# Performance work log

Measured on AMD Instinct MI355X. Metric: run time of the kernel, lower is better.

Reference implementation:

```python
import jax, jax.numpy as jnp
import numpy as np

B, L, D_IN, D_MODEL, D_STATE, N_LAYERS = 16, 2048, 64, 512, 16, 4
LN_EPS = 1e-5


def setup_inputs() -> dict:
    key = jax.random.key(0)
    ks = jax.random.split(key, 16)
    s = 0.02
    x = jax.random.normal(ks[0], (B, L, D_IN), jnp.float32)
    W_in0 = jax.random.normal(ks[1], (D_IN, D_MODEL), jnp.float32) * s
    b_in0 = jnp.zeros((D_MODEL,), jnp.float32)
    W_in = jax.random.normal(ks[2], (N_LAYERS - 1, D_MODEL, D_MODEL), jnp.float32) * s
    b_in = jnp.zeros((N_LAYERS - 1, D_MODEL), jnp.float32)
    # S4D-style init: A_log = log(1..N) per channel
    A_log = jnp.broadcast_to(jnp.log(jnp.arange(1, D_STATE + 1, dtype=jnp.float32)), (N_LAYERS, D_MODEL, D_STATE)).copy()
    D_skip = jnp.ones((N_LAYERS, D_MODEL), jnp.float32)
    W_dt = jax.random.normal(ks[3], (N_LAYERS, D_MODEL, D_MODEL), jnp.float32) * s
    b_dt = jnp.full((N_LAYERS, D_MODEL), -4.0, jnp.float32)  # small initial dt
    W_B = jax.random.normal(ks[4], (N_LAYERS, D_MODEL, D_STATE), jnp.float32) * s
    W_C = jax.random.normal(ks[5], (N_LAYERS, D_MODEL, D_STATE), jnp.float32) * s
    ln_g = jnp.ones((D_MODEL,), jnp.float32)
    ln_b = jnp.zeros((D_MODEL,), jnp.float32)
    head_w = jax.random.normal(ks[6], (D_MODEL, 1), jnp.float32) * s
    head_b = jnp.zeros((1,), jnp.float32)
    return {"x": x, "W_in0": W_in0, "b_in0": b_in0, "W_in": W_in, "b_in": b_in,
            "A_log": A_log, "D_skip": D_skip, "W_dt": W_dt, "b_dt": b_dt,
            "W_B": W_B, "W_C": W_C, "ln_g": ln_g, "ln_b": ln_b,
            "head_w": head_w, "head_b": head_b}


def _mamba_layer(x, W_in_l, b_in_l, A_log_l, D_l, W_dt_l, b_dt_l, W_B_l, W_C_l):
    # x: (B, L, d_in) -> y: (B, L, D_MODEL)
    u = x @ W_in_l + b_in_l                    # (B, L, D)
    dt = jax.nn.softplus(u @ W_dt_l + b_dt_l)  # (B, L, D)
    Bm = u @ W_B_l                             # (B, L, N)
    Cm = u @ W_C_l                             # (B, L, N)
    A = -jnp.exp(A_log_l)                      # (D, N)

    def step(h, inp):
        dt_t, u_t, B_t, C_t = inp              # (B,D),(B,D),(B,N),(B,N)
        dA = jnp.exp(dt_t[..., None] * A)      # (B, D, N)
        h = dA * h + (dt_t * u_t)[..., None] * B_t[:, None, :]
        y_t = jnp.einsum('bdn,bn->bd', h, C_t)
        return h, y_t

    h0 = jnp.zeros((u.shape[0], u.shape[2], A.shape[1]), u.dtype)
    xs = (jnp.swapaxes(dt, 0, 1), jnp.swapaxes(u, 0, 1),
          jnp.swapaxes(Bm, 0, 1), jnp.swapaxes(Cm, 0, 1))
    _, ys = jax.lax.scan(step, h0, xs)         # ys: (L, B, D)
    return jnp.swapaxes(ys, 0, 1) + u * D_l


def reference(x, W_in0, b_in0, W_in, b_in, A_log, D_skip, W_dt, b_dt, W_B, W_C, ln_g, ln_b, head_w, head_b):
    h = x
    for i in range(N_LAYERS):
        Wi = W_in0 if i == 0 else W_in[i - 1]
        bi = b_in0 if i == 0 else b_in[i - 1]
        h = _mamba_layer(h, Wi, bi, A_log[i], D_skip[i], W_dt[i], b_dt[i], W_B[i], W_C[i])
    # LayerNorm over d_model
    mu = jnp.mean(h, axis=-1, keepdims=True)
    var = jnp.mean(jnp.square(h - mu), axis=-1, keepdims=True)
    h = (h - mu) * jax.lax.rsqrt(var + LN_EPS) * ln_g + ln_b
    return h[:, -1, :] @ head_w + head_b       # (B, 1)
```

## Files before the change

kernel.cpp:

```cpp
#include <hip/hip_runtime.h>
#include <hip/hip_bf16.h>
#include <cstdint>
#include <cstddef>

#define B_SZ    16
#define L_SZ    2048
#define DIN     64
#define DMODEL  512
#define DSTATE  16
#define NLAYERS 4
#define LN_EPS  1e-5f
#define NC      32
#define TCH     (L_SZ / NC)
#define NFUSED  (2 * DMODEL)

typedef __bf16 bf16x8 __attribute__((ext_vector_type(8)));
typedef float  f32x4  __attribute__((ext_vector_type(4)));
typedef unsigned short u16;
typedef unsigned int   u32;

__device__ __forceinline__ u16 f2bf(float f) {
    u32 u = __builtin_bit_cast(u32, f);
    u += 0x7fffu + ((u >> 16) & 1u);
    return (u16)(u >> 16);
}
__device__ __forceinline__ float bf2f(u16 v) {
    u32 u = ((u32)v) << 16;
    return __builtin_bit_cast(float, u);
}

__device__ __forceinline__ void pow16(float q, float* a_) {
    float q2 = q * q, q4 = q2 * q2, q8 = q4 * q4;
    a_[0] = q;        a_[1] = q2;       a_[2] = q2 * q;   a_[3] = q4;
    a_[4] = q4 * q;   a_[5] = q4 * q2;  a_[6] = a_[5] * q; a_[7] = q8;
    a_[8] = q8 * q;   a_[9] = q8 * q2;  a_[10] = a_[9] * q; a_[11] = q8 * q4;
    a_[12] = a_[11] * q; a_[13] = a_[11] * q2; a_[14] = a_[13] * q; a_[15] = q8 * q8;
}

#define LOG2E 1.4426950408889634f

__device__ __forceinline__ void gload16(const void* g, void* l) {
    __builtin_amdgcn_global_load_lds(
        (__attribute__((address_space(1))) void*)(g),
        (__attribute__((address_space(3))) void*)(l), 16, 0, 0);
}

template <int K>
__global__ __launch_bounds__(256) void gemm_fused(
    const u16* __restrict__ A, const u16* __restrict__ BT,
    const float* __restrict__ bias, u16* __restrict__ Cu,
    u16* __restrict__ Cdt, int M)
{
    constexpr int BM = 128, BK = 64;
    constexpr int NT = K / BK;
    __shared__ u16 As[2][BM * BK];
    __shared__ u16 Bs[2][BM * BK];

    const int tid = threadIdx.x;
    const int wv = tid >> 6, ln = tid & 63;
    const int bm = blockIdx.x * BM, bn = blockIdx.y * BM;
    const int wm = (wv >> 1) * 64, wn = (wv & 1) * 64;

    f32x4 acc[4][4];
#pragma unroll
    for (int i = 0; i < 4; ++i)
#pragma unroll
        for (int j = 0; j < 4; ++j) acc[i][j] = (f32x4){0.f, 0.f, 0.f, 0.f};

    auto stage = [&](int buf, int k0) {
#pragma unroll
        for (int i = 0; i < 4; ++i) {
            int t = i * 256 + tid;
            int m = t >> 3, s = t & 7;
            int ksrc = (s ^ (m & 7)) * 8;
            gload16(A + (size_t)(bm + m) * K + k0 + ksrc,
                    &As[buf][(i * 256 + wv * 64) * 8]);
            gload16(BT + (size_t)(bn + m) * K + k0 + ksrc,
                    &Bs[buf][(i * 256 + wv * 64) * 8]);
        }
    };

    stage(0, 0);
    if (NT > 1) stage(1, BK);

#pragma unroll
    for (int kt = 0; kt < NT; ++kt) {
        if (kt == NT - 1) asm volatile("s_waitcnt vmcnt(0)" ::: "memory");
        else              asm volatile("s_waitcnt vmcnt(8)" ::: "memory");
        __builtin_amdgcn_s_barrier();

        const int buf = kt & 1;
#pragma unroll
        for (int ks = 0; ks < 2; ++ks) {
            bf16x8 af[4], bfr[4];
            const int g = ln >> 4, lm = ln & 15;
            const int c = ks * 4 + g;
#pragma unroll
            for (int f = 0; f < 4; ++f) {
                int ml = wm + f * 16 + lm;
                af[f] = *(const bf16x8*)&As[buf][ml * 64 + ((c ^ (ml & 7)) * 8)];
                int nl = wn + f * 16 + lm;
                bfr[f] = *(const bf16x8*)&Bs[buf][nl * 64 + ((c ^ (nl & 7)) * 8)];
            }
#pragma unroll
            for (int fm = 0; fm < 4; ++fm)
#pragma unroll
                for (int fn = 0; fn < 4; ++fn)
                    acc[fm][fn] = __builtin_amdgcn_mfma_f32_16x16x32_bf16(
                        af[fm], bfr[fn], acc[fm][fn], 0, 0, 0);
        }

        asm volatile("s_waitcnt lgkmcnt(0)" ::: "memory");
        __builtin_amdgcn_s_barrier();
        if (kt + 2 < NT) stage(buf, (kt + 2) * BK);
    }

    const int cg = ln >> 4, lc = ln & 15;
    const bool uside = (bn < DMODEL);
#pragma unroll
    for (int fm = 0; fm < 4; ++fm) {
#pragma unroll
        for (int fn = 0; fn < 4; ++fn) {
            int col = bn + wn + fn * 16 + lc;
            float bv = bias[col];
#pragma unroll
            for (int r = 0; r < 4; ++r) {
                int row = bm + wm + fm * 16 + cg * 4 + r;
                float v = acc[fm][fn][r] + bv;
                if (uside) {
                    Cu[(size_t)row * DMODEL + col] = f2bf(v);
                } else {
                    v = (v > 20.f) ? v : __logf(1.f + __expf(v));
                    Cdt[(size_t)row * DMODEL + (col - DMODEL)] = f2bf(v);
                }
            }
        }
    }
}

__global__ __launch_bounds__(256) void wtrans(
    const float* __restrict__ W, u16* __restrict__ WT, int K, int N)
{
    __shared__ float tile[32][33];
    int k0 = blockIdx.x * 32, n0 = blockIdx.y * 32;
    int tx = threadIdx.x & 31, ty = threadIdx.x >> 5;
#pragma unroll
    for (int i = 0; i < 4; ++i)
        tile[ty + 8 * i][tx] = W[(size_t)(k0 + ty + 8 * i) * N + n0 + tx];
    __syncthreads();
#pragma unroll
    for (int i = 0; i < 4; ++i)
        WT[(size_t)(n0 + ty + 8 * i) * K + k0 + tx] = f2bf(tile[tx][ty + 8 * i]);
}

__global__ __launch_bounds__(256) void wcombo(
    const float* __restrict__ Win,
    const float* __restrict__ Wdt,
    u16* __restrict__ outT,
    int KD)
{
    __shared__ float wi[16][516];
    __shared__ float wd[512][16];
    const int k0 = blockIdx.x * 16, n0 = blockIdx.y * 16;
    const int tid = threadIdx.x;
    for (int i = tid; i < 16 * 128; i += 256) {
        int r = i >> 7, c = i & 127;
        *(float4*)&wi[r][c * 4] =
            *(const float4*)&Win[(size_t)(k0 + r) * DMODEL + c * 4];
    }
    for (int i = tid; i < 512 * 4; i += 256) {
        int j = i >> 2, c = i & 3;
        *(float4*)&wd[j][c * 4] =
            *(const float4*)&Wdt[(size_t)j * DMODEL + n0 + c * 4];
    }
    __syncthreads();
    const int kk = tid & 15, nn = tid >> 4;
    float acc = 0.f;
#pragma unroll 8
    for (int j = 0; j < 512; ++j)
        acc = fmaf(wi[kk][j], wd[j][nn], acc);
    outT[(size_t)(n0 + nn) * KD + k0 + kk] = f2bf(acc);
}

__global__ __launch_bounds__(256) void biasprep(
    const float* __restrict__ bin, const float* __restrict__ Wdt,
    const float* __restrict__ bdt, float* __restrict__ biascat)
{
    int idx = blockIdx.x * 256 + threadIdx.x;
    if (idx < DMODEL) { biascat[idx] = bin[idx]; return; }
    int n = idx - DMODEL;
    float acc = bdt[n];
    for (int j = 0; j < DMODEL; ++j)
        acc = fmaf(bin[j], Wdt[(size_t)j * DMODEL + n], acc);
    biascat[idx] = acc;
}

__global__ __launch_bounds__(256) void castx(
    const float* __restrict__ x, u16* __restrict__ xb, int n4)
{
    int i = blockIdx.x * 256 + threadIdx.x;
    if (i < n4) {
        float4 v = ((const float4*)x)[i];
        ushort4 o;
        o.x = f2bf(v.x); o.y = f2bf(v.y); o.z = f2bf(v.z); o.w = f2bf(v.w);
        ((ushort4*)xb)[i] = o;
    }
}

__global__ __launch_bounds__(256) void prep_wbc(
    const float* __restrict__ WB, const float* __restrict__ WC,
    u16* __restrict__ WBCT)
{
    int idx = blockIdx.x * 256 + threadIdx.x;
    int l = idx >> 14;
    int r = idx & 16383;
    int n = r >> 9, k = r & 511;
    float v = (n < 16) ? WB[((size_t)l * DMODEL + k) * DSTATE + n]
                       : WC[((size_t)l * DMODEL + k) * DSTATE + (n - 16)];
    WBCT[((size_t)l * 32 + n) * DMODEL + k] = f2bf(v);
}

__global__ __launch_bounds__(256) void gemm_bc_mfma(
    const u16* __restrict__ A, const u16* __restrict__ WBCT,
    float* __restrict__ Bo, float* __restrict__ Co)
{
    const int tid = threadIdx.x;
    const int wv = tid >> 6, ln = tid & 63;
    const int m0 = blockIdx.x * 64 + wv * 16;
    const int g = ln >> 4, lm = ln & 15;

    f32x4 accB = (f32x4){0.f, 0.f, 0.f, 0.f};
    f32x4 accC = (f32x4){0.f, 0.f, 0.f, 0.f};
    const u16* arow = A + (size_t)(m0 + lm) * DMODEL;
    const u16* wb = WBCT + (size_t)lm * DMODEL;
    const u16* wc = WBCT + (size_t)(lm + 16) * DMODEL;
#pragma unroll
    for (int ks = 0; ks < DMODEL / 32; ++ks) {
        int ko = ks * 32 + g * 8;
        bf16x8 a = *(const bf16x8*)&arow[ko];
        bf16x8 b = *(const bf16x8*)&wb[ko];
        bf16x8 c = *(const bf16x8*)&wc[ko];
        accB = __builtin_amdgcn_mfma_f32_16x16x32_bf16(a, b, accB, 0, 0, 0);
        accC = __builtin_amdgcn_mfma_f32_16x16x32_bf16(a, c, accC, 0, 0, 0);
    }
#pragma unroll
    for (int r = 0; r < 4; ++r) {
        int m = m0 + g * 4 + r;
        Bo[(size_t)m * DSTATE + lm] = accB[r];
        Co[(size_t)m * DSTATE + lm] = accC[r];
    }
}

__global__ __launch_bounds__(256) void scan_pass1(
    const u16* __restrict__ u, const u16* __restrict__ dt,
    const float* __restrict__ Bm, const float* __restrict__ A_log,
    float* __restrict__ P, float* __restrict__ S)
{
    const int tid = threadIdx.x;
    const int d = blockIdx.x * 256 + tid;
    const int c = blockIdx.y, b = blockIdx.z;
    __shared__ float Bs[TCH][DSTATE];

    const float* Bsrc = Bm + ((size_t)b * L_SZ + (size_t)c * TCH) * DSTATE;
    for (int i = tid; i < TCH * DSTATE / 4; i += 256)
        ((float4*)Bs)[i] = ((const float4*)Bsrc)[i];

    float Ac[16];
#pragma unroll
    for (int n = 0; n < 16; ++n) Ac[n] = -__expf(A_log[d * DSTATE + n]);
    bool geo = true;
#pragma unroll
    for (int n = 1; n < 16; ++n)
        geo &= fabsf(Ac[n] - (n + 1) * Ac[0]) <= 1e-4f * (n + 1) * fabsf(Ac[0]);
    __syncthreads();

    float s[16];
#pragma unroll
    for (int n = 0; n < 16; ++n) s[n] = 0.f;

    const size_t base = ((size_t)b * L_SZ + (size_t)c * TCH) * DMODEL + d;
    size_t o = (((size_t)b * NC + c) * DMODEL + d) * DSTATE;

    if (geo) {
        const float cK = Ac[0] * LOG2E;
        float qp = 1.f;
#pragma unroll 2
        for (int t = 0; t < TCH; ++t) {
            float dtv = bf2f(dt[base + (size_t)t * DMODEL]);
            float uv  = bf2f(u [base + (size_t)t * DMODEL]);
            float du = dtv * uv;
            float q = exp2f(dtv * cK);
            qp *= q;
            float a_[16];
            pow16(q, a_);
#pragma unroll
            for (int n = 0; n < 16; ++n)
                s[n] = fmaf(a_[n], s[n], du * Bs[t][n]);
        }
        float p_[16];
        pow16(qp, p_);
#pragma unroll
        for (int n = 0; n < 16; ++n) { P[o + n] = p_[n]; S[o + n] = s[n]; }
    } else {
        float p[16];
#pragma unroll
        for (int n = 0; n < 16; ++n) p[n] = 1.f;
#pragma unroll 2
        for (int t = 0; t < TCH; ++t) {
            float dtv = bf2f(dt[base + (size_t)t * DMODEL]);
            float uv  = bf2f(u [base + (size_t)t * DMODEL]);
            float du = dtv * uv;
#pragma unroll
            for (int n = 0; n < 16; ++n) {
                float a = __expf(dtv * Ac[n]);
                p[n] *= a;
                s[n] = fmaf(a, s[n], du * Bs[t][n]);
            }
        }
#pragma unroll
        for (int n = 0; n < 16; ++n) { P[o + n] = p[n]; S[o + n] = s[n]; }
    }
}

__global__ __launch_bounds__(256) void scan_fix(
    const float* __restrict__ P, const float* __restrict__ S,
    float* __restrict__ H0)
{
    const int idx = blockIdx.x * 256 + threadIdx.x;
    const int dn = idx & (DMODEL * DSTATE - 1);
    const int b = idx >> 13;
    float h = 0.f;
#pragma unroll
    for (int c = 0; c < NC; ++c) {
        size_t o = (((size_t)b * NC + c) << 13) + dn;
        H0[o] = h;
        h = fmaf(P[o], h, S[o]);
    }
}

__global__ __launch_bounds__(256) void scan_pass2(
    const u16* __restrict__ u, const u16* __restrict__ dt,
    const float* __restrict__ Bm, const float* __restrict__ Cm,
    const float* __restrict__ A_log, const float* __restrict__ Dskip,
    const float* __restrict__ H0, u16* __restrict__ yb,
    float* __restrict__ ylast)
{
    const int tid = threadIdx.x;
    const int d = blockIdx.x * 256 + tid;
    const int c = blockIdx.y, b = blockIdx.z;
    __shared__ float Bs[TCH][DSTATE];
    __shared__ float Cs[TCH][DSTATE];

    const float* Bsrc = Bm + ((size_t)b * L_SZ + (size_t)c * TCH) * DSTATE;
    const float* Csrc = Cm + ((size_t)b * L_SZ + (size_t)c * TCH) * DSTATE;
    for (int i = tid; i < TCH * DSTATE / 4; i += 256) {
        ((float4*)Bs)[i] = ((const float4*)Bsrc)[i];
        ((float4*)Cs)[i] = ((const float4*)Csrc)[i];
    }

    float Ac[16];
#pragma unroll
    for (int n = 0; n < 16; ++n) Ac[n] = -__expf(A_log[d * DSTATE + n]);
    bool geo = true;
#pragma unroll
    for (int n = 1; n < 16; ++n)
        geo &= fabsf(Ac[n] - (n + 1) * Ac[0]) <= 1e-4f * (n + 1) * fabsf(Ac[0]);
    const float Dk = Dskip[d];

    float h[16];
    size_t ho = (((size_t)b * NC + c) * DMODEL + d) * DSTATE;
#pragma unroll
    for (int n = 0; n < 16; ++n) h[n] = H0[ho + n];
    __syncthreads();

    const size_t base = ((size_t)b * L_SZ + (size_t)c * TCH) * DMODEL + d;

    if (geo) {
        const float cK = Ac[0] * LOG2E;
#pragma unroll 2
        for (int t = 0; t < TCH; ++t) {
            float dtv = bf2f(dt[base + (size_t)t * DMODEL]);
            float uv  = bf2f(u [base + (size_t)t * DMODEL]);
            float du = dtv * uv;
            float q = exp2f(dtv * cK);
            float a_[16];
            pow16(q, a_);
            float yv = 0.f;
#pragma unroll
            for (int n = 0; n < 16; ++n) {
                h[n] = fmaf(a_[n], h[n], du * Bs[t][n]);
                yv = fmaf(h[n], Cs[t][n], yv);
            }
            yv = fmaf(uv, Dk, yv);
            yb[base + (size_t)t * DMODEL] = f2bf(yv);
            if (c == NC - 1 && t == TCH - 1) ylast[(size_t)b * DMODEL + d] = yv;
        }
    } else {
#pragma unroll 2
        for (int t = 0; t < TCH; ++t) {
            float dtv = bf2f(dt[base + (size_t)t * DMODEL]);
            float uv  = bf2f(u [base + (size_t)t * DMODEL]);
            float du = dtv * uv;
            float yv = 0.f;
#pragma unroll
            for (int n = 0; n < 16; ++n) {
                float a = __expf(dtv * Ac[n]);
                h[n] = fmaf(a, h[n], du * Bs[t][n]);
                yv = fmaf(h[n], Cs[t][n], yv);
            }
            yv = fmaf(uv, Dk, yv);
            yb[base + (size_t)t * DMODEL] = f2bf(yv);
            if (c == NC - 1 && t == TCH - 1) ylast[(size_t)b * DMODEL + d] = yv;
        }
    }
}

__global__ __launch_bounds__(256) void ln_head_kernel(
    const float* __restrict__ ylast, const float* __restrict__ g,
    const float* __restrict__ bb, const float* __restrict__ hw,
    const float* __restrict__ hb, float* __restrict__ out)
{
    const int b = blockIdx.x;
    const int tid = threadIdx.x;
    const float* row = ylast + (size_t)b * DMODEL;
    float v0 = row[tid], v1 = row[tid + 256];
    float s = v0 + v1;
    float s2 = v0 * v0 + v1 * v1;
#pragma unroll
    for (int o = 32; o >= 1; o >>= 1) {
        s += __shfl_xor(s, o);
        s2 += __shfl_xor(s2, o);
    }
    __shared__ float red[8];
    const int w = tid >> 6;
    if ((tid & 63) == 0) { red[w] = s; red[4 + w] = s2; }
    __syncthreads();
    s = red[0] + red[1] + red[2] + red[3];
    s2 = red[4] + red[5] + red[6] + red[7];
    float mu = s * (1.f / DMODEL);
    float var = s2 * (1.f / DMODEL) - mu * mu;
    float r = rsqrtf(var + LN_EPS);
    float c = ((v0 - mu) * r * g[tid] + bb[tid]) * hw[tid]
            + ((v1 - mu) * r * g[tid + 256] + bb[tid + 256]) * hw[tid + 256];
#pragma unroll
    for (int o = 32; o >= 1; o >>= 1) c += __shfl_xor(c, o);
    __syncthreads();
    if ((tid & 63) == 0) red[w] = c;
    __syncthreads();
    if (tid == 0) out[b] = red[0] + red[1] + red[2] + red[3] + hb[0];
}

extern "C" void kernel_launch(void* const* d_in, const int* in_sizes, int n_in,
                              void* d_out, int out_size, void* d_ws, size_t ws_size,
                              hipStream_t stream)
{
    const float* x      = (const float*)d_in[0];
    const float* W_in0  = (const float*)d_in[1];
    const float* b_in0  = (const float*)d_in[2];
    const float* W_in   = (const float*)d_in[3];
    const float* b_in   = (const float*)d_in[4];
    const float* A_log  = (const float*)d_in[5];
    const float* D_skip = (const float*)d_in[6];
    const float* W_dt   = (const float*)d_in[7];
    const float* b_dt   = (const float*)d_in[8];
    const float* W_B    = (const float*)d_in[9];
    const float* W_C    = (const float*)d_in[10];
    const float* ln_g   = (const float*)d_in[11];
    const float* ln_b   = (const float*)d_in[12];
    const float* head_w = (const float*)d_in[13];
    const float* head_b = (const float*)d_in[14];
    float* out = (float*)d_out;

    const size_t BLD = (size_t)B_SZ * L_SZ * DMODEL;
    const size_t BLN = (size_t)B_SZ * L_SZ * DSTATE;
    const size_t BCD = (size_t)B_SZ * NC * DMODEL * DSTATE;
    const size_t XBN = (size_t)B_SZ * L_SZ * DIN;

    float* fp = (float*)d_ws;
    float* Bbuf  = fp; fp += BLN;
    float* Cbuf  = fp; fp += BLN;
    float* Pbuf  = fp; fp += BCD;
    float* Sbuf  = fp; fp += BCD;
    float* H0buf = fp; fp += BCD;
    float* ylast = fp; fp += (size_t)B_SZ * DMODEL;
    float* biascat = fp; fp += (size_t)NLAYERS * NFUSED;
    u16* hp = (u16*)fp;
    u16* xb    = hp; hp += XBN;
    u16* ub    = hp; hp += BLD;
    u16* dtb   = hp; hp += BLD;
    u16* ybuf  = hp; hp += BLD;
    u16* BT0   = hp; hp += (size_t)NFUSED * DIN;
    u16* BTcat = hp; hp += (size_t)(NLAYERS - 1) * NFUSED * DMODEL;
    u16* WBCT  = hp; hp += (size_t)NLAYERS * 32 * DMODEL;

    const int M = B_SZ * L_SZ;

    castx<<<(XBN / 4 + 255) / 256, 256, 0, stream>>>(x, xb, XBN / 4);
    prep_wbc<<<(NLAYERS * 32 * DMODEL) / 256, 256, 0, stream>>>(W_B, W_C, WBCT);
    wtrans<<<dim3(DIN / 32, DMODEL / 32), 256, 0, stream>>>(W_in0, BT0, DIN, DMODEL);
    wcombo<<<dim3(DIN / 16, DMODEL / 16), 256, 0, stream>>>(
        W_in0, W_dt, BT0 + (size_t)DMODEL * DIN, DIN);
    biasprep<<<4, 256, 0, stream>>>(b_in0, W_dt, b_dt, biascat);
    for (int l = 1; l < NLAYERS; ++l) {
        u16* BTl = BTcat + (size_t)(l - 1) * NFUSED * DMODEL;
        const float* Wl = W_in + (size_t)(l - 1) * DMODEL * DMODEL;
        const float* Wd = W_dt + (size_t)l * DMODEL * DMODEL;
        wtrans<<<dim3(DMODEL / 32, DMODEL / 32), 256, 0, stream>>>(Wl, BTl, DMODEL, DMODEL);
        wcombo<<<dim3(DMODEL / 16, DMODEL / 16), 256, 0, stream>>>(
            Wl, Wd, BTl + (size_t)DMODEL * DMODEL, DMODEL);
        biasprep<<<4, 256, 0, stream>>>(
            b_in + (size_t)(l - 1) * DMODEL, Wd, b_dt + (size_t)l * DMODEL,
            biascat + (size_t)l * NFUSED);
    }

    for (int l = 0; l < NLAYERS; ++l) {
        if (l == 0) {
            gemm_fused<DIN><<<dim3(M / 128, NFUSED / 128), 256, 0, stream>>>(
                xb, BT0, biascat, ub, dtb, M);
        } else {
            gemm_fused<DMODEL><<<dim3(M / 128, NFUSED / 128), 256, 0, stream>>>(
                ybuf, BTcat + (size_t)(l - 1) * NFUSED * DMODEL,
                biascat + (size_t)l * NFUSED, ub, dtb, M);
        }
        gemm_bc_mfma<<<M / 64, 256, 0, stream>>>(
            ub, WBCT + (size_t)l * 32 * DMODEL, Bbuf, Cbuf);
        const float* Al = A_log + (size_t)l * DMODEL * DSTATE;
        scan_pass1<<<dim3(DMODEL / 256, NC, B_SZ), 256, 0, stream>>>(
            ub, dtb, Bbuf, Al, Pbuf, Sbuf);
        scan_fix<<<(B_SZ * DMODEL * DSTATE) / 256, 256, 0, stream>>>(
            Pbuf, Sbuf, H0buf);
        scan_pass2<<<dim3(DMODEL / 256, NC, B_SZ), 256, 0, stream>>>(
            ub, dtb, Bbuf, Cbuf, Al, D_skip + (size_t)l * DMODEL,
            H0buf, ybuf, ylast);
    }

    ln_head_kernel<<<B_SZ, 256, 0, stream>>>(ylast, ln_g, ln_b, head_w, head_b, out);
}
```

Before: 762.5 us.

## Use 512-thread GEMM blocks and batch per-layer weight prep launches

The fused input/dt GEMM now runs 8 waves per 128x128 tile, each computing a 32x64 sub-tile with half the accumulators. Staging is split across more threads, and the grid is flattened to a 1D index. The aim is more waves per tile to hide latency and lower register pressure, at the cost of fewer MFMAs per LDS fragment load. Separately, the per-layer weight transpose, combine and bias prep launches are folded into single launches using blockIdx.z, which cuts launch overhead.

```diff
diff --git a/kernel.cpp b/kernel.cpp
--- a/kernel.cpp
+++ b/kernel.cpp
@@ -46,7 +46,7 @@
 }
 
 template <int K>
-__global__ __launch_bounds__(256) void gemm_fused(
+__global__ __launch_bounds__(512) void gemm_fused(
     const u16* __restrict__ A, const u16* __restrict__ BT,
     const float* __restrict__ bias, u16* __restrict__ Cu,
     u16* __restrict__ Cdt, int M)
@@ -58,25 +58,26 @@
 
     const int tid = threadIdx.x;
     const int wv = tid >> 6, ln = tid & 63;
-    const int bm = blockIdx.x * BM, bn = blockIdx.y * BM;
-    const int wm = (wv >> 1) * 64, wn = (wv & 1) * 64;
-
-    f32x4 acc[4][4];
-#pragma unroll
-    for (int i = 0; i < 4; ++i)
+    const int mb = blockIdx.x & 255, nb = blockIdx.x >> 8;
+    const int bm = mb * BM, bn = nb * BM;
+    const int wm = (wv >> 1) * 32, wn = (wv & 1) * 64;
+
+    f32x4 acc[2][4];
+#pragma unroll
+    for (int i = 0; i < 2; ++i)
 #pragma unroll
         for (int j = 0; j < 4; ++j) acc[i][j] = (f32x4){0.f, 0.f, 0.f, 0.f};
 
     auto stage = [&](int buf, int k0) {
 #pragma unroll
-        for (int i = 0; i < 4; ++i) {
-            int t = i * 256 + tid;
+        for (int i = 0; i < 2; ++i) {
+            int t = i * 512 + tid;
             int m = t >> 3, s = t & 7;
             int ksrc = (s ^ (m & 7)) * 8;
             gload16(A + (size_t)(bm + m) * K + k0 + ksrc,
-                    &As[buf][(i * 256 + wv * 64) * 8]);
+                    &As[buf][(i * 512 + wv * 64) * 8]);
             gload16(BT + (size_t)(bn + m) * K + k0 + ksrc,
-                    &Bs[buf][(i * 256 + wv * 64) * 8]);
+                    &Bs[buf][(i * 512 + wv * 64) * 8]);
         }
     };
 
@@ -86,28 +87,31 @@
 #pragma unroll
     for (int kt = 0; kt < NT; ++kt) {
         if (kt == NT - 1) asm volatile("s_waitcnt vmcnt(0)" ::: "memory");
-        else              asm volatile("s_waitcnt vmcnt(8)" ::: "memory");
+        else              asm volatile("s_waitcnt vmcnt(4)" ::: "memory");
         __builtin_amdgcn_s_barrier();
 
         const int buf = kt & 1;
 #pragma unroll
         for (int ks = 0; ks < 2; ++ks) {
-            bf16x8 af[4], bfr[4];
+            bf16x8 af[2], bfr[4];
             const int g = ln >> 4, lm = ln & 15;
             const int c = ks * 4 + g;
 #pragma unroll
+            for (int e = 0; e < 2; ++e) {
+                int ml = wm + e * 16 + lm;
+                af[e] = *(const bf16x8*)&As[buf][ml * 64 + ((c ^ (ml & 7)) * 8)];
+            }
+#pragma unroll
             for (int f = 0; f < 4; ++f) {
-                int ml = wm + f * 16 + lm;
-                af[f] = *(const bf16x8*)&As[buf][ml * 64 + ((c ^ (ml & 7)) * 8)];
                 int nl = wn + f * 16 + lm;
                 bfr[f] = *(const bf16x8*)&Bs[buf][nl * 64 + ((c ^ (nl & 7)) * 8)];
             }
 #pragma unroll
-            for (int fm = 0; fm < 4; ++fm)
-#pragma unroll
-                for (int fn = 0; fn < 4; ++fn)
-                    acc[fm][fn] = __builtin_amdgcn_mfma_f32_16x16x32_bf16(
-                        af[fm], bfr[fn], acc[fm][fn], 0, 0, 0);
+            for (int e = 0; e < 2; ++e)
+#pragma unroll
+                for (int f = 0; f < 4; ++f)
+                    acc[e][f] = __builtin_amdgcn_mfma_f32_16x16x32_bf16(
+                        af[e], bfr[f], acc[e][f], 0, 0, 0);
         }
 
         asm volatile("s_waitcnt lgkmcnt(0)" ::: "memory");
@@ -118,15 +122,15 @@
     const int cg = ln >> 4, lc = ln & 15;
     const bool uside = (bn < DMODEL);
 #pragma unroll
-    for (int fm = 0; fm < 4; ++fm) {
-#pragma unroll
-        for (int fn = 0; fn < 4; ++fn) {
-            int col = bn + wn + fn * 16 + lc;
+    for (int e = 0; e < 2; ++e) {
+#pragma unroll
+        for (int f = 0; f < 4; ++f) {
+            int col = bn + wn + f * 16 + lc;
             float bv = bias[col];
 #pragma unroll
             for (int r = 0; r < 4; ++r) {
-                int row = bm + wm + fm * 16 + cg * 4 + r;
-                float v = acc[fm][fn][r] + bv;
+                int row = bm + wm + e * 16 + cg * 4 + r;
+                float v = acc[e][f][r] + bv;
                 if (uside) {
                     Cu[(size_t)row * DMODEL + col] = f2bf(v);
                 } else {
@@ -139,39 +143,44 @@
 }
 
 __global__ __launch_bounds__(256) void wtrans(
-    const float* __restrict__ W, u16* __restrict__ WT, int K, int N)
+    const float* __restrict__ W, u16* __restrict__ WT, int K, int N,
+    size_t inStride, size_t outStride)
 {
     __shared__ float tile[32][33];
+    const float* Wm = W + (size_t)blockIdx.z * inStride;
+    u16* WTm = WT + (size_t)blockIdx.z * outStride;
     int k0 = blockIdx.x * 32, n0 = blockIdx.y * 32;
     int tx = threadIdx.x & 31, ty = threadIdx.x >> 5;
 #pragma unroll
     for (int i = 0; i < 4; ++i)
-        tile[ty + 8 * i][tx] = W[(size_t)(k0 + ty + 8 * i) * N + n0 + tx];
+        tile[ty + 8 * i][tx] = Wm[(size_t)(k0 + ty + 8 * i) * N + n0 + tx];
     __syncthreads();
 #pragma unroll
     for (int i = 0; i < 4; ++i)
-        WT[(size_t)(n0 + ty + 8 * i) * K + k0 + tx] = f2bf(tile[tx][ty + 8 * i]);
+        WTm[(size_t)(n0 + ty + 8 * i) * K + k0 + tx] = f2bf(tile[tx][ty + 8 * i]);
 }
 
 __global__ __launch_bounds__(256) void wcombo(
-    const float* __restrict__ Win,
-    const float* __restrict__ Wdt,
-    u16* __restrict__ outT,
-    int KD)
+    const float* __restrict__ Win, const float* __restrict__ Wdt,
+    u16* __restrict__ outT, int KD,
+    size_t winStride, size_t wdtStride, size_t outStride)
 {
     __shared__ float wi[16][516];
     __shared__ float wd[512][16];
+    const float* WinL = Win + (size_t)blockIdx.z * winStride;
+    const float* WdtL = Wdt + (size_t)blockIdx.z * wdtStride;
+    u16* outL = outT + (size_t)blockIdx.z * outStride;
     const int k0 = blockIdx.x * 16, n0 = blockIdx.y * 16;
     const int tid = threadIdx.x;
     for (int i = tid; i < 16 * 128; i += 256) {
         int r = i >> 7, c = i & 127;
         *(float4*)&wi[r][c * 4] =
-            *(const float4*)&Win[(size_t)(k0 + r) * DMODEL + c * 4];
+            *(const float4*)&WinL[(size_t)(k0 + r) * DMODEL + c * 4];
     }
     for (int i = tid; i < 512 * 4; i += 256) {
         int j = i >> 2, c = i & 3;
         *(float4*)&wd[j][c * 4] =
-            *(const float4*)&Wdt[(size_t)j * DMODEL + n0 + c * 4];
+            *(const float4*)&WdtL[(size_t)j * DMODEL + n0 + c * 4];
     }
     __syncthreads();
     const int kk = tid & 15, nn = tid >> 4;
@@ -179,20 +188,25 @@
 #pragma unroll 8
     for (int j = 0; j < 512; ++j)
         acc = fmaf(wi[kk][j], wd[j][nn], acc);
-    outT[(size_t)(n0 + nn) * KD + k0 + kk] = f2bf(acc);
+    outL[(size_t)(n0 + nn) * KD + k0 + kk] = f2bf(acc);
 }
 
 __global__ __launch_bounds__(256) void biasprep(
     const float* __restrict__ bin, const float* __restrict__ Wdt,
-    const float* __restrict__ bdt, float* __restrict__ biascat)
-{
+    const float* __restrict__ bdt, float* __restrict__ biascat,
+    size_t binStride, size_t wdtStride, size_t bdtStride, size_t outStride)
+{
+    const float* binL = bin + (size_t)blockIdx.z * binStride;
+    const float* WdtL = Wdt + (size_t)blockIdx.z * wdtStride;
+    const float* bdtL = bdt + (size_t)blockIdx.z * bdtStride;
+    float* outL = biascat + (size_t)blockIdx.z * outStride;
     int idx = blockIdx.x * 256 + threadIdx.x;
-    if (idx < DMODEL) { biascat[idx] = bin[idx]; return; }
+    if (idx < DMODEL) { outL[idx] = binL[idx]; return; }
     int n = idx - DMODEL;
-    float acc = bdt[n];
+    float acc = bdtL[n];
     for (int j = 0; j < DMODEL; ++j)
-        acc = fmaf(bin[j], Wdt[(size_t)j * DMODEL + n], acc);
-    biascat[idx] = acc;
+        acc = fmaf(binL[j], WdtL[(size_t)j * DMODEL + n], acc);
+    outL[idx] = acc;
 }
 
 __global__ __launch_bounds__(256) void castx(
@@ -497,28 +511,30 @@
 
     castx<<<(XBN / 4 + 255) / 256, 256, 0, stream>>>(x, xb, XBN / 4);
     prep_wbc<<<(NLAYERS * 32 * DMODEL) / 256, 256, 0, stream>>>(W_B, W_C, WBCT);
-    wtrans<<<dim3(DIN / 32, DMODEL / 32), 256, 0, stream>>>(W_in0, BT0, DIN, DMODEL);
-    wcombo<<<dim3(DIN / 16, DMODEL / 16), 256, 0, stream>>>(
-        W_in0, W_dt, BT0 + (size_t)DMODEL * DIN, DIN);
-    biasprep<<<4, 256, 0, stream>>>(b_in0, W_dt, b_dt, biascat);
-    for (int l = 1; l < NLAYERS; ++l) {
-        u16* BTl = BTcat + (size_t)(l - 1) * NFUSED * DMODEL;
-        const float* Wl = W_in + (size_t)(l - 1) * DMODEL * DMODEL;
-        const float* Wd = W_dt + (size_t)l * DMODEL * DMODEL;
-        wtrans<<<dim3(DMODEL / 32, DMODEL / 32), 256, 0, stream>>>(Wl, BTl, DMODEL, DMODEL);
-        wcombo<<<dim3(DMODEL / 16, DMODEL / 16), 256, 0, stream>>>(
-            Wl, Wd, BTl + (size_t)DMODEL * DMODEL, DMODEL);
-        biasprep<<<4, 256, 0, stream>>>(
-            b_in + (size_t)(l - 1) * DMODEL, Wd, b_dt + (size_t)l * DMODEL,
-            biascat + (size_t)l * NFUSED);
-    }
+    wtrans<<<dim3(DIN / 32, DMODEL / 32, 1), 256, 0, stream>>>(
+        W_in0, BT0, DIN, DMODEL, 0, 0);
+    wcombo<<<dim3(DIN / 16, DMODEL / 16, 1), 256, 0, stream>>>(
+        W_in0, W_dt, BT0 + (size_t)DMODEL * DIN, DIN, 0, 0, 0);
+    biasprep<<<dim3(4, 1, 1), 256, 0, stream>>>(
+        b_in0, W_dt, b_dt, biascat, 0, 0, 0, 0);
+    wtrans<<<dim3(DMODEL / 32, DMODEL / 32, NLAYERS - 1), 256, 0, stream>>>(
+        W_in, BTcat, DMODEL, DMODEL,
+        (size_t)DMODEL * DMODEL, (size_t)NFUSED * DMODEL);
+    wcombo<<<dim3(DMODEL / 16, DMODEL / 16, NLAYERS - 1), 256, 0, stream>>>(
+        W_in, W_dt + (size_t)DMODEL * DMODEL,
+        BTcat + (size_t)DMODEL * DMODEL, DMODEL,
+        (size_t)DMODEL * DMODEL, (size_t)DMODEL * DMODEL,
+        (size_t)NFUSED * DMODEL);
+    biasprep<<<dim3(4, 1, NLAYERS - 1), 256, 0, stream>>>(
+        b_in, W_dt + (size_t)DMODEL * DMODEL, b_dt + DMODEL, biascat + NFUSED,
+        DMODEL, (size_t)DMODEL * DMODEL, DMODEL, NFUSED);
 
     for (int l = 0; l < NLAYERS; ++l) {
         if (l == 0) {
-            gemm_fused<DIN><<<dim3(M / 128, NFUSED / 128), 256, 0, stream>>>(
+            gemm_fused<DIN><<<(M / 128) * (NFUSED / 128), 512, 0, stream>>>(
                 xb, BT0, biascat, ub, dtb, M);
         } else {
-            gemm_fused<DMODEL><<<dim3(M / 128, NFUSED / 128), 256, 0, stream>>>(
+            gemm_fused<DMODEL><<<(M / 128) * (NFUSED / 128), 512, 0, stream>>>(
                 ybuf, BTcat + (size_t)(l - 1) * NFUSED * DMODEL,
                 biascat + (size_t)l * NFUSED, ub, dtb, M);
         }
```

New measurement: 700.8 us. 8.1% less time.
